# Optimization experiments

Hardware: AMD Instinct MI355X
Metric: run time of the kernel (lower is better)

## Reference

```python
import jax, jax.numpy as jnp
import numpy as np

N_NODES = 50000
N_EDGES = 800000
D_IN = 96
HID = 96
D_OUT = 64
NUM_LAYERS = 6  # conv1 + (NUM_LAYERS-2) hidden convs + out_conv


def gcn_conv(x, W, b, src, dst, n):
    """PyG GCNConv: add self-loops, symmetric D^-1/2 (A+I) D^-1/2 normalization."""
    h = x @ W  # [n, out_dim]
    loops = jnp.arange(n, dtype=src.dtype)
    s = jnp.concatenate([src, loops])
    d = jnp.concatenate([dst, loops])
    deg = jax.ops.segment_sum(jnp.ones_like(s, dtype=h.dtype), d, num_segments=n)
    dinv = jnp.where(deg > 0, jax.lax.rsqrt(deg), 0.0)
    norm = dinv[s] * dinv[d]                 # [E+n]
    msg = h[s] * norm[:, None]               # gather + scale
    out = jax.ops.segment_sum(msg, d, num_segments=n)  # scatter-add to targets
    return out + b


def setup_inputs() -> dict:
    key = jax.random.key(0)
    ks = jax.random.split(key, 10)
    x = jax.random.normal(ks[0], (N_NODES, D_IN), dtype=jnp.float32)
    edge_index = jax.random.randint(ks[1], (2, N_EDGES), 0, N_NODES, dtype=jnp.int32)
    ricci_curvature = jax.random.normal(ks[2], (N_EDGES,), dtype=jnp.float32)
    n_hidden = NUM_LAYERS - 2
    W1 = jax.random.normal(ks[3], (D_IN, HID), dtype=jnp.float32) * 0.05
    b1 = jnp.zeros((HID,), dtype=jnp.float32)
    Ws = jax.random.normal(ks[4], (n_hidden, HID, HID), dtype=jnp.float32) * 0.05
    bs = jnp.zeros((n_hidden, HID), dtype=jnp.float32)
    Wout = jax.random.normal(ks[5], ((NUM_LAYERS - 1) * HID, D_OUT), dtype=jnp.float32) * 0.05
    bout = jnp.zeros((D_OUT,), dtype=jnp.float32)
    return {
        "x": x, "edge_index": edge_index, "percent": 70,
        "ricci_curvature": ricci_curvature,
        "W1": W1, "b1": b1, "Ws": Ws, "bs": bs, "Wout": Wout, "bout": bout,
    }


def reference(x, edge_index, percent, ricci_curvature, W1, b1, Ws, bs, Wout, bout):
    # Eval path: no sampling / dynamic reweighting, dropout is identity, no BN.
    del percent, ricci_curvature
    n = x.shape[0]
    src, dst = edge_index[0], edge_index[1]
    res = []
    h = jax.nn.relu(gcn_conv(x, W1, b1, src, dst, n))
    res.append(h)
    for i in range(Ws.shape[0]):
        h = jax.nn.relu(gcn_conv(h, Ws[i], bs[i], src, dst, n))
        res.append(h)
    x_cat = jnp.concatenate(res, axis=1)  # JK concatenation: [n, (L-1)*HID]
    out = gcn_conv(x_cat, Wout, bout, src, dst, n)
    return (out,) + tuple(res)
```

## Files before the change

### kernel.cpp

```cpp
#include <hip/hip_runtime.h>


typedef unsigned short ushortT;
typedef __attribute__((ext_vector_type(8))) short bf16x8;
typedef __attribute__((ext_vector_type(4))) float f32x4;

__device__ __forceinline__ ushortT f2b(float f) {
    union { float f; unsigned int u; } v;
    v.f = f;
    unsigned int lsb = (v.u >> 16) & 1u;
    v.u += 0x7fffu + lsb;
    return (ushortT)(v.u >> 16);
}
__device__ __forceinline__ float b2f(ushortT u) {
    union { float f; unsigned int u; } v;
    v.u = ((unsigned int)u) << 16;
    return v.f;
}

__global__ void tw_kernel(const float* __restrict__ W, ushortT* __restrict__ Wt,
                          int K, int C) {
    int i = blockIdx.x * blockDim.x + threadIdx.x;
    if (i < K * C) {
        int c = i / K, k = i - c * K;
        Wt[i] = f2b(W[(size_t)k * C + c]);
    }
}

__global__ void count_kernel(const int* __restrict__ dst, int* __restrict__ degi, int E) {
    int e = blockIdx.x * blockDim.x + threadIdx.x;
    if (e < E) atomicAdd(&degi[dst[e]], 1);
}

__global__ void scan1(const int* __restrict__ degi, int* __restrict__ row_start,
                      int* __restrict__ partials, int n) {
    __shared__ int tmp[256];
    const int t = threadIdx.x;
    const int i = blockIdx.x * 256 + t;
    int val = (i < n) ? degi[i] : 0;
    tmp[t] = val;
    __syncthreads();
    for (int off = 1; off < 256; off <<= 1) {
        int v = (t >= off) ? tmp[t - off] : 0;
        __syncthreads();
        tmp[t] += v;
        __syncthreads();
    }
    if (i < n) row_start[i] = tmp[t] - val;
    if (t == 255) partials[blockIdx.x] = tmp[255];
}

__global__ void scan2(int* __restrict__ partials, int nb) {
    __shared__ int tmp[256];
    const int t = threadIdx.x;
    int val = (t < nb) ? partials[t] : 0;
    tmp[t] = val;
    __syncthreads();
    for (int off = 1; off < 256; off <<= 1) {
        int v = (t >= off) ? tmp[t - off] : 0;
        __syncthreads();
        tmp[t] += v;
        __syncthreads();
    }
    if (t < nb) partials[t] = tmp[t] - val;
}

__global__ void scan3(const int* __restrict__ degi, int* __restrict__ row_start,
                      const int* __restrict__ partials, float* __restrict__ dinv,
                      int n, int E) {
    const int i = blockIdx.x * 256 + threadIdx.x;
    if (i < n) {
        row_start[i] += partials[blockIdx.x];
        dinv[i] = rsqrtf((float)degi[i] + 1.0f);
    }
    if (i == 0) row_start[n] = E;
}

__global__ void fill_kernel(const int* __restrict__ src, const int* __restrict__ dst,
                            const int* __restrict__ row_start, int* __restrict__ degi,
                            int* __restrict__ col, int E) {
    int e = blockIdx.x * blockDim.x + threadIdx.x;
    if (e < E) {
        int d = dst[e];
        int pos = row_start[d] + atomicSub(&degi[d], 1) - 1;
        col[pos] = src[e];
    }
}

template <typename TIN>
__global__ __launch_bounds__(256) void gemm96_mfma(const TIN* __restrict__ X,
                                                   const ushortT* __restrict__ Wt,
                                                   const float* __restrict__ dinv,
                                                   ushortT* __restrict__ g, int n) {
    __shared__ __attribute__((aligned(16))) ushortT Xl[64][104];
    __shared__ __attribute__((aligned(16))) ushortT Wtl[96][104];
    const int tid = threadIdx.x;
    const int wave = tid >> 6, lane = tid & 63;
    const int quad = lane >> 4, m = lane & 15;
    const int row_base = blockIdx.x * 64;
    for (int i = tid; i < 96 * 24; i += 256) {
        int r = i / 24, c4 = (i % 24) * 4;
        *(ushort4*)&Wtl[r][c4] = *(const ushort4*)&Wt[r * 96 + c4];
    }
    for (int i = tid; i < 64 * 24; i += 256) {
        int r = i / 24, c4 = (i % 24) * 4;
        int grow = min(row_base + r, n - 1);
        if constexpr (sizeof(TIN) == 4) {
            float4 v = *(const float4*)&X[(size_t)grow * 96 + c4];
            ushort4 o = {f2b(v.x), f2b(v.y), f2b(v.z), f2b(v.w)};
            *(ushort4*)&Xl[r][c4] = o;
        } else {
            *(ushort4*)&Xl[r][c4] = *(const ushort4*)&X[(size_t)grow * 96 + c4];
        }
    }
    __syncthreads();
    f32x4 acc[6] = {};
#pragma unroll
    for (int ks = 0; ks < 3; ++ks) {
        bf16x8 a = *(bf16x8*)&Xl[wave * 16 + m][ks * 32 + quad * 8];
#pragma unroll
        for (int ct = 0; ct < 6; ++ct) {
            bf16x8 b = *(bf16x8*)&Wtl[ct * 16 + m][ks * 32 + quad * 8];
            acc[ct] = __builtin_amdgcn_mfma_f32_16x16x32_bf16(a, b, acc[ct], 0, 0, 0);
        }
    }
    float di[4];
    int rows[4];
#pragma unroll
    for (int r = 0; r < 4; ++r) {
        rows[r] = row_base + wave * 16 + quad * 4 + r;
        di[r] = (rows[r] < n) ? dinv[rows[r]] : 0.f;
    }
#pragma unroll
    for (int ct = 0; ct < 6; ++ct) {
        int colx = ct * 16 + m;
#pragma unroll
        for (int r = 0; r < 4; ++r)
            if (rows[r] < n) g[(size_t)rows[r] * 96 + colx] = f2b(acc[ct][r] * di[r]);
    }
}

__global__ __launch_bounds__(256) void gemm_out_mfma(const float* __restrict__ hcat,
                                                     const ushortT* __restrict__ Wt,
                                                     const float* __restrict__ dinv,
                                                     ushortT* __restrict__ g, int n) {
    __shared__ __attribute__((aligned(16))) ushortT Xl[64][104];
    __shared__ __attribute__((aligned(16))) ushortT Wtl[64][104];
    const int tid = threadIdx.x;
    const int wave = tid >> 6, lane = tid & 63;
    const int quad = lane >> 4, m = lane & 15;
    const int row_base = blockIdx.x * 64;
    f32x4 acc[4] = {};
    for (int seg = 0; seg < 5; ++seg) {
        const float* hl = hcat + (size_t)seg * (size_t)n * 96;
        __syncthreads();
        for (int i = tid; i < 64 * 24; i += 256) {
            int r = i / 24, c4 = (i % 24) * 4;
            *(ushort4*)&Wtl[r][c4] = *(const ushort4*)&Wt[r * 480 + seg * 96 + c4];
        }
        for (int i = tid; i < 64 * 24; i += 256) {
            int r = i / 24, c4 = (i % 24) * 4;
            int grow = min(row_base + r, n - 1);
            float4 v = *(const float4*)&hl[(size_t)grow * 96 + c4];
            ushort4 o = {f2b(v.x), f2b(v.y), f2b(v.z), f2b(v.w)};
            *(ushort4*)&Xl[r][c4] = o;
        }
        __syncthreads();
#pragma unroll
        for (int ks = 0; ks < 3; ++ks) {
            bf16x8 a = *(bf16x8*)&Xl[wave * 16 + m][ks * 32 + quad * 8];
#pragma unroll
            for (int ct = 0; ct < 4; ++ct) {
                bf16x8 b = *(bf16x8*)&Wtl[ct * 16 + m][ks * 32 + quad * 8];
                acc[ct] = __builtin_amdgcn_mfma_f32_16x16x32_bf16(a, b, acc[ct], 0, 0, 0);
            }
        }
    }
    float di[4];
    int rows[4];
#pragma unroll
    for (int r = 0; r < 4; ++r) {
        rows[r] = row_base + wave * 16 + quad * 4 + r;
        di[r] = (rows[r] < n) ? dinv[rows[r]] : 0.f;
    }
#pragma unroll
    for (int ct = 0; ct < 4; ++ct) {
        int colx = ct * 16 + m;
#pragma unroll
        for (int r = 0; r < 4; ++r)
            if (rows[r] < n) g[(size_t)rows[r] * 64 + colx] = f2b(acc[ct][r] * di[r]);
    }
}

template <int F, bool RELU, bool WRITE_BF16>
__global__ void agg_csr(const int* __restrict__ row_start, const int* __restrict__ col,
                        const ushortT* __restrict__ g, const float* __restrict__ dinv,
                        const float* __restrict__ b, float* __restrict__ out,
                        ushortT* __restrict__ hb, int n) {
    constexpr int NV = F / 4;
    const int lane = threadIdx.x & 63;
    const int half = lane >> 5;
    const int l32 = lane & 31;
    const int v = blockIdx.x * (blockDim.x >> 6) + (threadIdx.x >> 6);
    if (v >= n) return;
    const int e0 = row_start[v];
    const int e1 = row_start[v + 1];
    const bool act = (l32 < NV);
    float a0 = 0.f, a1 = 0.f, a2 = 0.f, a3 = 0.f;
    if (half == 0 && act) {
        ushort4 s = *(const ushort4*)&g[(size_t)v * F + l32 * 4];
        a0 = b2f(s.x); a1 = b2f(s.y); a2 = b2f(s.z); a3 = b2f(s.w);
    }
    int e = e0 + half;
    for (; e + 2 < e1; e += 4) {
        int c0 = col[e], c1 = col[e + 2];
        if (act) {
            ushort4 g0 = *(const ushort4*)&g[(size_t)c0 * F + l32 * 4];
            ushort4 g1 = *(const ushort4*)&g[(size_t)c1 * F + l32 * 4];
            a0 += b2f(g0.x) + b2f(g1.x);
            a1 += b2f(g0.y) + b2f(g1.y);
            a2 += b2f(g0.z) + b2f(g1.z);
            a3 += b2f(g0.w) + b2f(g1.w);
        }
    }
    for (; e < e1; e += 2) {
        int c = col[e];
        if (act) {
            ushort4 g0 = *(const ushort4*)&g[(size_t)c * F + l32 * 4];
            a0 += b2f(g0.x); a1 += b2f(g0.y); a2 += b2f(g0.z); a3 += b2f(g0.w);
        }
    }
    a0 += __shfl_xor(a0, 32);
    a1 += __shfl_xor(a1, 32);
    a2 += __shfl_xor(a2, 32);
    a3 += __shfl_xor(a3, 32);
    if (half == 0 && act) {
        const float di = dinv[v];
        float4 r;
        r.x = a0 * di + b[l32 * 4 + 0];
        r.y = a1 * di + b[l32 * 4 + 1];
        r.z = a2 * di + b[l32 * 4 + 2];
        r.w = a3 * di + b[l32 * 4 + 3];
        if (RELU) {
            r.x = fmaxf(r.x, 0.f); r.y = fmaxf(r.y, 0.f);
            r.z = fmaxf(r.z, 0.f); r.w = fmaxf(r.w, 0.f);
        }
        *(float4*)&out[(size_t)v * F + l32 * 4] = r;
        if (WRITE_BF16) {
            ushort4 o = {f2b(r.x), f2b(r.y), f2b(r.z), f2b(r.w)};
            *(ushort4*)&hb[(size_t)v * F + l32 * 4] = o;
        }
    }
}

extern "C" void kernel_launch(void* const* d_in, const int* in_sizes, int n_in,
                              void* d_out, int out_size, void* d_ws, size_t ws_size,
                              hipStream_t stream) {
    const float* x    = (const float*)d_in[0];
    const int*   ei   = (const int*)d_in[1];
    const float* W1   = (const float*)d_in[4];
    const float* b1   = (const float*)d_in[5];
    const float* Wsl  = (const float*)d_in[6];
    const float* bsl  = (const float*)d_in[7];
    const float* Wout = (const float*)d_in[8];
    const float* bout = (const float*)d_in[9];

    const int n = in_sizes[0] / 96;
    const int E = in_sizes[1] / 2;
    const int* src = ei;
    const int* dst = ei + E;

    int*     degi      = (int*)d_ws;
    int*     row_start = degi + n;
    int*     partials  = row_start + n + 1;
    int*     col       = partials + 256;
    float*   dinv      = (float*)(col + E);
    ushortT* g         = (ushortT*)(dinv + n);
    ushortT* hb        = g + (size_t)n * 96;
    ushortT* wt1       = hb + (size_t)n * 96;
    ushortT* wts       = wt1 + 96 * 96;
    ushortT* wto       = wts + 4 * 96 * 96;

    float* out  = (float*)d_out;
    float* hseg = out + (size_t)n * 64;

    const int nthr = 256;
    const int gE   = (E + nthr - 1) / nthr;
    const int gAgg = (n + 3) / 4;
    const int gT64 = (n + 63) / 64;
    const int nb   = (n + 255) / 256;

    tw_kernel<<<(96 * 96 + 255) / 256, 256, 0, stream>>>(W1, wt1, 96, 96);
    for (int l = 0; l < 4; ++l)
        tw_kernel<<<(96 * 96 + 255) / 256, 256, 0, stream>>>(
            Wsl + (size_t)l * 96 * 96, wts + (size_t)l * 96 * 96, 96, 96);
    tw_kernel<<<(480 * 64 + 255) / 256, 256, 0, stream>>>(Wout, wto, 480, 64);

    hipMemsetAsync(degi, 0, (size_t)n * sizeof(int), stream);
    count_kernel<<<gE, nthr, 0, stream>>>(dst, degi, E);
    scan1<<<nb, 256, 0, stream>>>(degi, row_start, partials, n);
    scan2<<<1, 256, 0, stream>>>(partials, nb);
    scan3<<<nb, 256, 0, stream>>>(degi, row_start, partials, dinv, n, E);
    fill_kernel<<<gE, nthr, 0, stream>>>(src, dst, row_start, degi, col, E);

    gemm96_mfma<float><<<gT64, 256, 0, stream>>>(x, wt1, dinv, g, n);
    agg_csr<96, true, true><<<gAgg, nthr, 0, stream>>>(row_start, col, g, dinv, b1,
                                                       hseg, hb, n);

    for (int l = 0; l < 4; ++l) {
        float* hnext = hseg + (size_t)(l + 1) * (size_t)n * 96;
        gemm96_mfma<ushortT><<<gT64, 256, 0, stream>>>(hb, wts + (size_t)l * 96 * 96,
                                                       dinv, g, n);
        agg_csr<96, true, true><<<gAgg, nthr, 0, stream>>>(row_start, col, g, dinv,
                                                           bsl + (size_t)l * 96, hnext, hb, n);
    }

    gemm_out_mfma<<<gT64, 256, 0, stream>>>(hseg, wto, dinv, g, n);
    agg_csr<64, false, false><<<gAgg, nthr, 0, stream>>>(row_start, col, g, dinv, bout,
                                                         out, nullptr, n);
}
```

Before: 571.6 us.

## Fuse weight prep with degree zeroing, keep bf16 layer copies, unroll aggregation

Merges the six weight-transpose launches and the degree memset into one prep kernel. When the workspace is large enough, each layer's bf16 activation copy goes to its own buffer so the output GEMM reads bf16 instead of re-reading and converting fp32 concatenated features. The CSR aggregation loop is unrolled to four gathers per iteration with split accumulators to expose more memory-level parallelism, and the bias is read with a vector load. The cost is extra workspace and a runtime branch on workspace size.

```diff
diff --git a/kernel.cpp b/kernel.cpp
--- a/kernel.cpp
+++ b/kernel.cpp
@@ -18,12 +18,28 @@
     return v.f;
 }
 
-__global__ void tw_kernel(const float* __restrict__ W, ushortT* __restrict__ Wt,
-                          int K, int C) {
+__global__ void prep_kernel(const float* __restrict__ W1, const float* __restrict__ Wsl,
+                            const float* __restrict__ Wout, ushortT* __restrict__ wt1,
+                            ushortT* __restrict__ wts, ushortT* __restrict__ wto,
+                            int* __restrict__ degi, int n) {
+    const int SQ = 96 * 96;
+    const int T1 = 5 * SQ;
+    const int T2 = T1 + 480 * 64;
     int i = blockIdx.x * blockDim.x + threadIdx.x;
-    if (i < K * C) {
-        int c = i / K, k = i - c * K;
-        Wt[i] = f2b(W[(size_t)k * C + c]);
+    if (i < T1) {
+        int l = i / SQ, j = i - l * SQ;
+        int c = j / 96, k = j - c * 96;
+        if (l == 0)
+            wt1[j] = f2b(W1[k * 96 + c]);
+        else
+            wts[(size_t)(l - 1) * SQ + j] = f2b(Wsl[(size_t)(l - 1) * SQ + k * 96 + c]);
+    } else if (i < T2) {
+        int j = i - T1;
+        int c = j / 480, k = j - c * 480;
+        wto[j] = f2b(Wout[(size_t)k * 64 + c]);
+    } else {
+        int j = i - T2;
+        if (j < n) degi[j] = 0;
     }
 }
 
@@ -140,7 +156,8 @@
     }
 }
 
-__global__ __launch_bounds__(256) void gemm_out_mfma(const float* __restrict__ hcat,
+template <typename TIN>
+__global__ __launch_bounds__(256) void gemm_out_mfma(const TIN* __restrict__ hcat,
                                                      const ushortT* __restrict__ Wt,
                                                      const float* __restrict__ dinv,
                                                      ushortT* __restrict__ g, int n) {
@@ -152,7 +169,7 @@
     const int row_base = blockIdx.x * 64;
     f32x4 acc[4] = {};
     for (int seg = 0; seg < 5; ++seg) {
-        const float* hl = hcat + (size_t)seg * (size_t)n * 96;
+        const TIN* hl = hcat + (size_t)seg * (size_t)n * 96;
         __syncthreads();
         for (int i = tid; i < 64 * 24; i += 256) {
             int r = i / 24, c4 = (i % 24) * 4;
@@ -161,9 +178,13 @@
         for (int i = tid; i < 64 * 24; i += 256) {
             int r = i / 24, c4 = (i % 24) * 4;
             int grow = min(row_base + r, n - 1);
-            float4 v = *(const float4*)&hl[(size_t)grow * 96 + c4];
-            ushort4 o = {f2b(v.x), f2b(v.y), f2b(v.z), f2b(v.w)};
-            *(ushort4*)&Xl[r][c4] = o;
+            if constexpr (sizeof(TIN) == 4) {
+                float4 v = *(const float4*)&hl[(size_t)grow * 96 + c4];
+                ushort4 o = {f2b(v.x), f2b(v.y), f2b(v.z), f2b(v.w)};
+                *(ushort4*)&Xl[r][c4] = o;
+            } else {
+                *(ushort4*)&Xl[r][c4] = *(const ushort4*)&hl[(size_t)grow * 96 + c4];
+            }
         }
         __syncthreads();
 #pragma unroll
@@ -206,17 +227,32 @@
     const int e0 = row_start[v];
     const int e1 = row_start[v + 1];
     const bool act = (l32 < NV);
+    const size_t fo = (size_t)l32 * 4;
     float a0 = 0.f, a1 = 0.f, a2 = 0.f, a3 = 0.f;
+    float s0 = 0.f, s1 = 0.f, s2 = 0.f, s3 = 0.f;
     if (half == 0 && act) {
-        ushort4 s = *(const ushort4*)&g[(size_t)v * F + l32 * 4];
+        ushort4 s = *(const ushort4*)&g[(size_t)v * F + fo];
         a0 = b2f(s.x); a1 = b2f(s.y); a2 = b2f(s.z); a3 = b2f(s.w);
     }
     int e = e0 + half;
+    for (; e + 6 < e1; e += 8) {
+        int c0 = col[e], c1 = col[e + 2], c2 = col[e + 4], c3 = col[e + 6];
+        if (act) {
+            ushort4 g0 = *(const ushort4*)&g[(size_t)c0 * F + fo];
+            ushort4 g1 = *(const ushort4*)&g[(size_t)c1 * F + fo];
+            ushort4 g2 = *(const ushort4*)&g[(size_t)c2 * F + fo];
+            ushort4 g3 = *(const ushort4*)&g[(size_t)c3 * F + fo];
+            a0 += b2f(g0.x) + b2f(g1.x); s0 += b2f(g2.x) + b2f(g3.x);
+            a1 += b2f(g0.y) + b2f(g1.y); s1 += b2f(g2.y) + b2f(g3.y);
+            a2 += b2f(g0.z) + b2f(g1.z); s2 += b2f(g2.z) + b2f(g3.z);
+            a3 += b2f(g0.w) + b2f(g1.w); s3 += b2f(g2.w) + b2f(g3.w);
+        }
+    }
     for (; e + 2 < e1; e += 4) {
         int c0 = col[e], c1 = col[e + 2];
         if (act) {
-            ushort4 g0 = *(const ushort4*)&g[(size_t)c0 * F + l32 * 4];
-            ushort4 g1 = *(const ushort4*)&g[(size_t)c1 * F + l32 * 4];
+            ushort4 g0 = *(const ushort4*)&g[(size_t)c0 * F + fo];
+            ushort4 g1 = *(const ushort4*)&g[(size_t)c1 * F + fo];
             a0 += b2f(g0.x) + b2f(g1.x);
             a1 += b2f(g0.y) + b2f(g1.y);
             a2 += b2f(g0.z) + b2f(g1.z);
@@ -226,21 +262,23 @@
     for (; e < e1; e += 2) {
         int c = col[e];
         if (act) {
-            ushort4 g0 = *(const ushort4*)&g[(size_t)c * F + l32 * 4];
+            ushort4 g0 = *(const ushort4*)&g[(size_t)c * F + fo];
             a0 += b2f(g0.x); a1 += b2f(g0.y); a2 += b2f(g0.z); a3 += b2f(g0.w);
         }
     }
+    a0 += s0; a1 += s1; a2 += s2; a3 += s3;
     a0 += __shfl_xor(a0, 32);
     a1 += __shfl_xor(a1, 32);
     a2 += __shfl_xor(a2, 32);
     a3 += __shfl_xor(a3, 32);
     if (half == 0 && act) {
         const float di = dinv[v];
+        const float4 bv = *(const float4*)&b[l32 * 4];
         float4 r;
-        r.x = a0 * di + b[l32 * 4 + 0];
-        r.y = a1 * di + b[l32 * 4 + 1];
-        r.z = a2 * di + b[l32 * 4 + 2];
-        r.w = a3 * di + b[l32 * 4 + 3];
+        r.x = a0 * di + bv.x;
+        r.y = a1 * di + bv.y;
+        r.z = a2 * di + bv.z;
+        r.w = a3 * di + bv.w;
         if (RELU) {
             r.x = fmaxf(r.x, 0.f); r.y = fmaxf(r.y, 0.f);
             r.z = fmaxf(r.z, 0.f); r.w = fmaxf(r.w, 0.f);
@@ -270,16 +308,23 @@
     const int* src = ei;
     const int* dst = ei + E;
 
-    int*     degi      = (int*)d_ws;
-    int*     row_start = degi + n;
-    int*     partials  = row_start + n + 1;
-    int*     col       = partials + 256;
-    float*   dinv      = (float*)(col + E);
-    ushortT* g         = (ushortT*)(dinv + n);
-    ushortT* hb        = g + (size_t)n * 96;
-    ushortT* wt1       = hb + (size_t)n * 96;
-    ushortT* wts       = wt1 + 96 * 96;
-    ushortT* wto       = wts + 4 * 96 * 96;
+    char* p = (char*)d_ws;
+    int*     degi      = (int*)p;              p += (size_t)n * 4;
+    int*     row_start = (int*)p;              p += (size_t)(n + 1) * 4;
+    int*     partials  = (int*)p;              p += 256 * 4;
+    int*     col       = (int*)p;              p += (size_t)E * 4;
+    float*   dinv      = (float*)p;            p += (size_t)n * 4;
+    ushortT* g         = (ushortT*)p;          p += (size_t)n * 96 * 2;
+    ushortT* hball     = (ushortT*)p;
+    const size_t wbytes = (size_t)(5 * 9216 + 30720) * 2;
+    const size_t fixed  = (size_t)(p - (char*)d_ws);
+    const bool   big    = (fixed + (size_t)5 * n * 96 * 2 + wbytes) <= ws_size;
+    const size_t hbsz   = big ? (size_t)5 * n * 96 : (size_t)n * 96;
+    p += hbsz * 2;
+    ushortT* wt1 = (ushortT*)p;
+    ushortT* wts = wt1 + 5 * 9216 - 4 * 9216;
+    wts = wt1 + 9216;
+    ushortT* wto = wts + 4 * 9216;
 
     float* out  = (float*)d_out;
     float* hseg = out + (size_t)n * 64;
@@ -290,32 +335,36 @@
     const int gT64 = (n + 63) / 64;
     const int nb   = (n + 255) / 256;
 
-    tw_kernel<<<(96 * 96 + 255) / 256, 256, 0, stream>>>(W1, wt1, 96, 96);
-    for (int l = 0; l < 4; ++l)
-        tw_kernel<<<(96 * 96 + 255) / 256, 256, 0, stream>>>(
-            Wsl + (size_t)l * 96 * 96, wts + (size_t)l * 96 * 96, 96, 96);
-    tw_kernel<<<(480 * 64 + 255) / 256, 256, 0, stream>>>(Wout, wto, 480, 64);
-
-    hipMemsetAsync(degi, 0, (size_t)n * sizeof(int), stream);
+    const int prep_items = 76800 + n;
+    prep_kernel<<<(prep_items + 255) / 256, 256, 0, stream>>>(W1, Wsl, Wout, wt1, wts,
+                                                              wto, degi, n);
+
     count_kernel<<<gE, nthr, 0, stream>>>(dst, degi, E);
     scan1<<<nb, 256, 0, stream>>>(degi, row_start, partials, n);
     scan2<<<1, 256, 0, stream>>>(partials, nb);
     scan3<<<nb, 256, 0, stream>>>(degi, row_start, partials, dinv, n, E);
     fill_kernel<<<gE, nthr, 0, stream>>>(src, dst, row_start, degi, col, E);
 
+    ushortT* hb0 = hball;
     gemm96_mfma<float><<<gT64, 256, 0, stream>>>(x, wt1, dinv, g, n);
     agg_csr<96, true, true><<<gAgg, nthr, 0, stream>>>(row_start, col, g, dinv, b1,
-                                                       hseg, hb, n);
+                                                       hseg, hb0, n);
 
     for (int l = 0; l < 4; ++l) {
-        float* hnext = hseg + (size_t)(l + 1) * (size_t)n * 96;
-        gemm96_mfma<ushortT><<<gT64, 256, 0, stream>>>(hb, wts + (size_t)l * 96 * 96,
+        float*   hnext = hseg + (size_t)(l + 1) * (size_t)n * 96;
+        ushortT* hbin  = big ? (hball + (size_t)l * n * 96) : hball;
+        ushortT* hbout = big ? (hball + (size_t)(l + 1) * n * 96) : hball;
+        gemm96_mfma<ushortT><<<gT64, 256, 0, stream>>>(hbin, wts + (size_t)l * 9216,
                                                        dinv, g, n);
         agg_csr<96, true, true><<<gAgg, nthr, 0, stream>>>(row_start, col, g, dinv,
-                                                           bsl + (size_t)l * 96, hnext, hb, n);
-    }
-
-    gemm_out_mfma<<<gT64, 256, 0, stream>>>(hseg, wto, dinv, g, n);
+                                                           bsl + (size_t)l * 96, hnext,
+                                                           hbout, n);
+    }
+
+    if (big)
+        gemm_out_mfma<ushortT><<<gT64, 256, 0, stream>>>(hball, wto, dinv, g, n);
+    else
+        gemm_out_mfma<float><<<gT64, 256, 0, stream>>>(hseg, wto, dinv, g, n);
     agg_csr<64, false, false><<<gAgg, nthr, 0, stream>>>(row_start, col, g, dinv, bout,
                                                          out, nullptr, n);
 }
```

After: 523.9 us. -8.3%, faster.
